# Performance work log

Hardware: AMD Instinct MI355X
Metric: run time of the kernel (lower is better)

## Reference

```python
import jax, jax.numpy as jnp
import numpy as np

B, T, D, H = 2, 2048, 1024, 16
DK = D // H  # 64


def setup_inputs() -> dict:
    key = jax.random.key(0)
    ks = jax.random.split(key, 13)
    s = 1.0 / np.sqrt(D)
    return {
        "x": jax.random.normal(ks[0], (B, T, D), jnp.float32),
        "Wq_w": jax.random.normal(ks[1], (D, D), jnp.float32) * s,
        "Wq_b": jax.random.normal(ks[2], (D,), jnp.float32) * 0.01,
        "Wk_w": jax.random.normal(ks[3], (D, D), jnp.float32) * s,
        "Wk_b": jax.random.normal(ks[4], (D,), jnp.float32) * 0.01,
        "Wv_w": jax.random.normal(ks[5], (D, D), jnp.float32) * s,
        "Wv_b": jax.random.normal(ks[6], (D,), jnp.float32) * 0.01,
        "Wo_w": jax.random.normal(ks[7], (D, D), jnp.float32) * s,
        "Wo_b": jax.random.normal(ks[8], (D,), jnp.float32) * 0.01,
        "qr": jax.random.normal(ks[9], (B, H, T, DK), jnp.float32),
        "qi": jax.random.normal(ks[10], (B, H, T, DK), jnp.float32),
        "kr": jax.random.normal(ks[11], (B, H, T, DK), jnp.float32),
        "ki": jax.random.normal(ks[12], (B, H, T, DK), jnp.float32),
    }


def _heads(y):
    # [B,T,D] -> [B,H,T,DK]
    return y.reshape(B, T, H, DK).transpose(0, 2, 1, 3)


def reference(x, Wq_w, Wq_b, Wk_w, Wk_b, Wv_w, Wv_b, Wo_w, Wo_b, qr, qi, kr, ki):
    Q = _heads(x @ Wq_w.T + Wq_b)
    K = _heads(x @ Wk_w.T + Wk_b)
    V = _heads(x @ Wv_w.T + Wv_b)
    # quantum noise: sin(atan2(imag, real))
    Q = Q + jnp.sin(jnp.arctan2(qi, qr))
    K = K + jnp.sin(jnp.arctan2(ki, kr))
    # Recursive fractal attention collapses: branches are identical and
    # deterministic, so (A1+A2)/2 == depth-0 attention at every level.
    scores = jnp.einsum("bhtd,bhsd->bhts", Q, K) / np.sqrt(DK).astype(np.float32)
    weights = jax.nn.softmax(scores, axis=-1)
    attn = jnp.einsum("bhts,bhsd->bhtd", weights, V)  # [B,H,T,DK]
    out = attn.transpose(0, 2, 1, 3).reshape(B, T, D)
    return out @ Wo_w.T + Wo_b
```

## Files before the change

### kernel.cpp

```cpp
#include <hip/hip_runtime.h>
#include <hip/hip_fp16.h>
#include <stdint.h>

typedef _Float16 half_t;
typedef _Float16 hf2 __attribute__((ext_vector_type(2)));
typedef _Float16 hf4 __attribute__((ext_vector_type(4)));
typedef _Float16 hf8 __attribute__((ext_vector_type(8)));
typedef float f32x16 __attribute__((ext_vector_type(16)));
typedef unsigned uint2_t __attribute__((ext_vector_type(2)));

#define LOG2E 1.4426950408889634f

__device__ __forceinline__ void gload16(const void* g, void* l) {
  __builtin_amdgcn_global_load_lds(
      (const __attribute__((address_space(1))) unsigned int*)g,
      (__attribute__((address_space(3))) unsigned int*)l, 16, 0, 0);
}

__device__ __forceinline__ unsigned packrtz(float a, float b) {
  auto h = __builtin_amdgcn_cvt_pkrtz(a, b);
  union { decltype(h) h2; unsigned u; } c;
  c.h2 = h;
  return c.u;
}

__device__ __forceinline__ float exp2fast(float x) {
#if __has_builtin(__builtin_amdgcn_exp2f)
  return __builtin_amdgcn_exp2f(x);
#else
  return exp2f(x);
#endif
}

__device__ __forceinline__ float psum2(unsigned pw, hf2 ones, float acc) {
#if __has_builtin(__builtin_amdgcn_fdot2)
  union { unsigned u; hf2 h; } c;
  c.u = pw;
  return __builtin_amdgcn_fdot2(c.h, ones, acc, false);
#else
  union { unsigned u; hf2 h; } c;
  c.u = pw;
  return acc + (float)c.h[0] + (float)c.h[1];
#endif
}

__global__ __launch_bounds__(256) void cvt_kernel(
    const float* __restrict__ x, const float* __restrict__ wq,
    const float* __restrict__ wk, const float* __restrict__ wv,
    const float* __restrict__ wo, half_t* __restrict__ xh,
    half_t* __restrict__ wh) {
  long e = ((long)blockIdx.x * 256 + threadIdx.x) * 16;
  const float* src;
  half_t* dst;
  if (e < 4194304L) {
    src = x + e;
    dst = xh + e;
  } else {
    long j = e - 4194304L;
    int w = (int)(j >> 20);
    long off = j & 1048575L;
    src = (w == 0 ? wq : w == 1 ? wk : w == 2 ? wv : wo) + off;
    dst = wh + ((long)w << 20) + off;
  }
  const float4* s4 = (const float4*)src;
  float4 f0 = s4[0], f1 = s4[1], f2 = s4[2], f3 = s4[3];
  hf8 o0 = {(half_t)f0.x, (half_t)f0.y, (half_t)f0.z, (half_t)f0.w,
            (half_t)f1.x, (half_t)f1.y, (half_t)f1.z, (half_t)f1.w};
  hf8 o1 = {(half_t)f2.x, (half_t)f2.y, (half_t)f2.z, (half_t)f2.w,
            (half_t)f3.x, (half_t)f3.y, (half_t)f3.z, (half_t)f3.w};
  *(hf8*)dst = o0;
  *(hf8*)(dst + 8) = o1;
}

template <int CUR>
__device__ __forceinline__ void gstep(bool stage, const half_t* __restrict__ A,
                                      const half_t* __restrict__ Bt, char* ldsb,
                                      int wid, int& goA, int& goB, int aof0,
                                      int aof1, int aof2, int aof3, int bof0,
                                      int bof1, int bof2, int bof3,
                                      f32x16 acc[2]) {
  if (stage) {
#pragma unroll
    for (int i = 0; i < 4; i++)
      gload16(A + goA + i * 32768,
              ldsb + (CUR ^ 1) * 16384 + i * 4096 + wid * 1024);
#pragma unroll
    for (int i = 0; i < 2; i++)
      gload16(Bt + goB + i * 32768,
              ldsb + 32768 + (CUR ^ 1) * 8192 + i * 4096 + wid * 1024);
    goA += 64;
    goB += 64;
  }
  constexpr int ca = CUR * 16384;
  constexpr int cb = 32768 + CUR * 8192;
#pragma unroll
  for (int kc = 0; kc < 4; kc++) {
    const int ao = (kc == 0 ? aof0 : kc == 1 ? aof1 : kc == 2 ? aof2 : aof3);
    const int bo = (kc == 0 ? bof0 : kc == 1 ? bof1 : kc == 2 ? bof2 : bof3);
    hf8 af0 = *(const hf8*)(ldsb + ca + ao);
    hf8 af1 = *(const hf8*)(ldsb + ca + ao + 4096);
    hf8 bf = *(const hf8*)(ldsb + cb + bo);
    acc[0] = __builtin_amdgcn_mfma_f32_32x32x16_f16(af0, bf, acc[0], 0, 0, 0);
    acc[1] = __builtin_amdgcn_mfma_f32_32x32x16_f16(af1, bf, acc[1], 0, 0, 0);
  }
  __syncthreads();
}

__device__ __forceinline__ void gemm_core(const half_t* __restrict__ A,
                                          const half_t* __restrict__ Bt,
                                          int m0, int n0, char* ldsb,
                                          f32x16 acc[2]) {
  const int tid = threadIdx.x;
  const int wid = tid >> 6;
  const int lane = tid & 63;
  const int l31 = lane & 31;
  const int hh = lane >> 5;
  const int wm = wid >> 1, wn = wid & 1;

#pragma unroll
  for (int mt = 0; mt < 2; mt++)
#pragma unroll
    for (int i = 0; i < 16; i++) acc[mt][i] = 0.f;

  const int rowb = tid >> 3;
  const int c16 = (tid & 7) ^ (rowb & 7);
  int goA = (m0 + rowb) * 1024 + c16 * 8;
  int goB = (n0 + rowb) * 1024 + c16 * 8;

  const int swz0 = (hh * 16) ^ ((l31 & 7) << 4);
  const int swz1 = (32 + hh * 16) ^ ((l31 & 7) << 4);
  const int swz2 = (64 + hh * 16) ^ ((l31 & 7) << 4);
  const int swz3 = (96 + hh * 16) ^ ((l31 & 7) << 4);
  const int arow = (wm * 64 + l31) * 128;
  const int brow = (wn * 32 + l31) * 128;
  const int aof0 = arow + swz0, aof1 = arow + swz1, aof2 = arow + swz2,
            aof3 = arow + swz3;
  const int bof0 = brow + swz0, bof1 = brow + swz1, bof2 = brow + swz2,
            bof3 = brow + swz3;

#pragma unroll
  for (int i = 0; i < 4; i++)
    gload16(A + goA + i * 32768, ldsb + i * 4096 + wid * 1024);
#pragma unroll
  for (int i = 0; i < 2; i++)
    gload16(Bt + goB + i * 32768, ldsb + 32768 + i * 4096 + wid * 1024);
  goA += 64;
  goB += 64;
  __syncthreads();

  for (int kp = 0; kp < 8; ++kp) {
    gstep<0>(true, A, Bt, ldsb, wid, goA, goB, aof0, aof1, aof2, aof3, bof0,
             bof1, bof2, bof3, acc);
    gstep<1>(kp < 7, A, Bt, ldsb, wid, goA, goB, aof0, aof1, aof2, aof3, bof0,
             bof1, bof2, bof3, acc);
  }
}

__global__ __launch_bounds__(256, 3) void proj_kernel(
    const half_t* __restrict__ xh, const half_t* __restrict__ wh,
    const float* __restrict__ bq, const float* __restrict__ bk,
    const float* __restrict__ bv, const float* __restrict__ qr,
    const float* __restrict__ qi, const float* __restrict__ kr,
    const float* __restrict__ ki, half_t* __restrict__ Qh,
    half_t* __restrict__ Kh, half_t* __restrict__ Vth) {
  __shared__ __align__(16) char ldsb[49152];
  const int z = blockIdx.z;
  const half_t* Bt = wh + (size_t)z * 1048576;
  const int m0 = blockIdx.x * 128, n0 = blockIdx.y * 64;
  f32x16 acc[2];
  gemm_core(xh, Bt, m0, n0, ldsb, acc);

  const int tid = threadIdx.x;
  const int wid = tid >> 6;
  const int lane = tid & 63;
  const int l31 = lane & 31;
  const int hh = lane >> 5;
  const int wm = wid >> 1, wn = wid & 1;
  const float* bias = (z == 0) ? bq : (z == 1) ? bk : bv;
  const float* nr = (z == 0) ? qr : kr;
  const float* ni = (z == 0) ? qi : ki;
  const float scale = (z == 0) ? (0.125f * LOG2E) : 1.0f;

  const int n = n0 + wn * 32 + l31;
  const float bsv = bias[n];
  const int hd = n >> 6, d = n & 63;
#pragma unroll
  for (int mt = 0; mt < 2; mt++) {
    const int mbase = m0 + wm * 64 + mt * 32;
    if (z == 2) {
#pragma unroll
      for (int g = 0; g < 4; g++) {
        const int m = mbase + 8 * g + 4 * hh;
        const int bb = m >> 11, tt = m & 2047;
        hf4 pk;
#pragma unroll
        for (int i2 = 0; i2 < 4; i2++)
          pk[i2] = (half_t)(acc[mt][4 * g + i2] + bsv);
        *(hf4*)(Vth + (((size_t)(bb * 16 + hd) * 64 + d) * 2048 + tt)) = pk;
      }
    } else {
      half_t* dstp = (z == 0) ? Qh : Kh;
#pragma unroll
      for (int r = 0; r < 16; r++) {
        const int m = mbase + (r & 3) + 8 * (r >> 2) + 4 * hh;
        const int bb = m >> 11, tt = m & 2047;
        const size_t idx = ((size_t)(bb * 16 + hd) * 2048 + tt) * 64 + d;
        float v = acc[mt][r] + bsv;
        const float a_ = nr[idx], b_ = ni[idx];
        v += b_ * rsqrtf(a_ * a_ + b_ * b_);
        dstp[idx] = (half_t)(v * scale);
      }
    }
  }
}

template <int CUR>
__device__ __forceinline__ void attn_tile_t(
    bool stage, const half_t* __restrict__ Kb, const half_t* __restrict__ Vb,
    char* base, int qw, int& gk0, int& gk1, int& gv0, int& gv1,
    const int kofs[4], const hf8 qf[4], const f32x16& zv, f32x16 ot[2],
    float& psAcc, hf2 ones) {
  if (stage) {
    gload16(Kb + gk0, base + (CUR ^ 1) * 8192 + qw * 1024);
    gload16(Kb + gk1, base + (CUR ^ 1) * 8192 + 4096 + qw * 1024);
    gload16(Vb + gv0, base + 16384 + (CUR ^ 1) * 8192 + qw * 1024);
    gload16(Vb + gv1, base + 16384 + (CUR ^ 1) * 8192 + 4096 + qw * 1024);
    gk0 += 4096;
    gk1 += 4096;
    gv0 += 64;
    gv1 += 64;
  }
#pragma unroll
  for (int kt = 0; kt < 2; kt++) {
    __builtin_amdgcn_s_setprio(1);
    f32x16 s = __builtin_amdgcn_mfma_f32_32x32x16_f16(
        *(const hf8*)(base + kofs[0] + CUR * 8192 + kt * 4096), qf[0], zv, 0, 0,
        0);
    s = __builtin_amdgcn_mfma_f32_32x32x16_f16(
        *(const hf8*)(base + kofs[1] + CUR * 8192 + kt * 4096), qf[1], s, 0, 0,
        0);
    s = __builtin_amdgcn_mfma_f32_32x32x16_f16(
        *(const hf8*)(base + kofs[2] + CUR * 8192 + kt * 4096), qf[2], s, 0, 0,
        0);
    s = __builtin_amdgcn_mfma_f32_32x32x16_f16(
        *(const hf8*)(base + kofs[3] + CUR * 8192 + kt * 4096), qf[3], s, 0, 0,
        0);
    __builtin_amdgcn_s_setprio(0);

    unsigned pw[8];
#pragma unroll
    for (int j = 0; j < 8; j++) {
      float p0 = exp2fast(s[2 * j]);
      float p1 = exp2fast(s[2 * j + 1]);
      pw[j] = packrtz(p0, p1);
      psAcc = psum2(pw[j], ones, psAcc);
    }

#pragma unroll
    for (int sub = 0; sub < 2; sub++) {
      const int kc = kt * 2 + sub;
      unsigned a0 = pw[sub * 4 + 0], a1 = pw[sub * 4 + 1];
      unsigned a2 = pw[sub * 4 + 2], a3 = pw[sub * 4 + 3];
      union { unsigned u[4]; hf8 v; } pu;
#if __has_builtin(__builtin_amdgcn_permlane32_swap)
      uint2_t r02 = __builtin_amdgcn_permlane32_swap(a0, a2, false, false);
      uint2_t r13 = __builtin_amdgcn_permlane32_swap(a1, a3, false, false);
      pu.u[0] = r02[0];
      pu.u[1] = r13[0];
      pu.u[2] = r02[1];
      pu.u[3] = r13[1];
#else
      const int hh_ = (threadIdx.x & 63) >> 5;
      unsigned x0 = __shfl_xor(a0, 32, 64), x1 = __shfl_xor(a1, 32, 64);
      unsigned x2 = __shfl_xor(a2, 32, 64), x3 = __shfl_xor(a3, 32, 64);
      pu.u[0] = hh_ ? x2 : a0;
      pu.u[1] = hh_ ? x3 : a1;
      pu.u[2] = hh_ ? a2 : x0;
      pu.u[3] = hh_ ? a3 : x1;
#endif
      __builtin_amdgcn_s_setprio(1);
#pragma unroll
      for (int dt = 0; dt < 2; dt++) {
        hf8 vf =
            *(const hf8*)(base + kofs[kc] + 16384 + CUR * 8192 + dt * 4096);
        ot[dt] =
            __builtin_amdgcn_mfma_f32_32x32x16_f16(vf, pu.v, ot[dt], 0, 0, 0);
      }
      __builtin_amdgcn_s_setprio(0);
    }
  }
  __syncthreads();
}

__global__ __launch_bounds__(512, 4) void attn_kernel(
    const half_t* __restrict__ Qh, const half_t* __restrict__ Kh,
    const half_t* __restrict__ Vth, half_t* __restrict__ ah) {
  __shared__ __align__(16) char smem[65536];
  const int tid = threadIdx.x, wid = tid >> 6, lane = tid & 63;
  const int l31 = lane & 31, hh = lane >> 5;
  const int qw = wid & 3, g = wid >> 2;
  const int lin = blockIdx.x;
  const int slot = lin >> 3;
  const int bh = (lin & 7) * 4 + (slot >> 4);
  const int qb = slot & 15;
  const int b = bh >> 4, hd = bh & 15;
  const int t = qb * 128 + qw * 32 + l31;

  char* base = smem + g * 32768;

  const half_t* qrow = Qh + ((size_t)bh * 2048 + t) * 64;
  hf8 qf[4];
#pragma unroll
  for (int kc = 0; kc < 4; kc++) qf[kc] = *(const hf8*)(qrow + kc * 16 + hh * 8);

  f32x16 ot[2];
#pragma unroll
  for (int dt = 0; dt < 2; dt++)
#pragma unroll
    for (int i = 0; i < 16; i++) ot[dt][i] = 0.f;
  f32x16 zv;
#pragma unroll
  for (int i = 0; i < 16; i++) zv[i] = 0.f;
  float psAcc = 0.f;
  const hf2 ones = {(_Float16)1.0f, (_Float16)1.0f};

  const half_t* Kb = Kh + (size_t)bh * 2048 * 64;
  const half_t* Vb = Vth + (size_t)bh * 64 * 2048;
  const int kvbase = g * 1024;

  int kofs[4];
#pragma unroll
  for (int kc = 0; kc < 4; kc++)
    kofs[kc] = l31 * 128 + ((kc * 32 + hh * 16) ^ ((l31 & 7) << 4));

  int gk0, gk1, gv0, gv1;
  {
    int c0 = qw * 64 + lane, c1 = 256 + qw * 64 + lane;
    int r0 = c0 >> 3, s0 = (c0 & 7) ^ (r0 & 7);
    int r1 = c1 >> 3, s1 = (c1 & 7) ^ (r1 & 7);
    gk0 = (kvbase + r0) * 64 + s0 * 8;
    gk1 = (kvbase + r1) * 64 + s1 * 8;
    gv0 = r0 * 2048 + kvbase + s0 * 8;
    gv1 = r1 * 2048 + kvbase + s1 * 8;
  }
  gload16(Kb + gk0, base + qw * 1024);
  gload16(Kb + gk1, base + 4096 + qw * 1024);
  gload16(Vb + gv0, base + 16384 + qw * 1024);
  gload16(Vb + gv1, base + 16384 + 4096 + qw * 1024);
  gk0 += 4096;
  gk1 += 4096;
  gv0 += 64;
  gv1 += 64;
  __syncthreads();

  for (int tp = 0; tp < 8; ++tp) {
    attn_tile_t<0>(true, Kb, Vb, base, qw, gk0, gk1, gv0, gv1, kofs, qf, zv,
                   ot, psAcc, ones);
    attn_tile_t<1>(tp < 7, Kb, Vb, base, qw, gk0, gk1, gv0, gv1, kofs, qf, zv,
                   ot, psAcc, ones);
  }

  const float lrun = psAcc + __shfl_xor(psAcc, 32, 64);

  float* cb = (float*)smem;
  float* lb = (float*)(smem + 32768);
  if (g == 1) {
#pragma unroll
    for (int dt = 0; dt < 2; dt++)
#pragma unroll
      for (int i = 0; i < 16; i++)
        cb[((qw * 2 + dt) * 16 + i) * 64 + lane] = ot[dt][i];
    lb[qw * 64 + lane] = lrun;
  }
  __syncthreads();
  if (g == 0) {
#pragma unroll
    for (int dt = 0; dt < 2; dt++)
#pragma unroll
      for (int i = 0; i < 16; i++)
        ot[dt][i] += cb[((qw * 2 + dt) * 16 + i) * 64 + lane];
    const float inv = 1.0f / (lrun + lb[qw * 64 + lane]);
    const size_t obase = ((size_t)b * 2048 + t) * 1024 + hd * 64;
#pragma unroll
    for (int dt = 0; dt < 2; dt++)
#pragma unroll
      for (int gg = 0; gg < 4; gg++) {
        hf4 pk;
#pragma unroll
        for (int i2 = 0; i2 < 4; i2++)
          pk[i2] = (half_t)(ot[dt][4 * gg + i2] * inv);
        *(hf4*)(ah + obase + dt * 32 + 8 * gg + 4 * hh) = pk;
      }
  }
}

__global__ __launch_bounds__(256, 3) void outproj_kernel(
    const half_t* __restrict__ ah, const half_t* __restrict__ woh,
    const float* __restrict__ bo, float* __restrict__ out) {
  __shared__ __align__(16) char ldsb[49152];
  const int m0 = blockIdx.x * 128, n0 = blockIdx.y * 64;
  f32x16 acc[2];
  gemm_core(ah, woh, m0, n0, ldsb, acc);
  const int tid = threadIdx.x, wid = tid >> 6, lane = tid & 63;
  const int l31 = lane & 31, hh = lane >> 5;
  const int wm = wid >> 1, wn = wid & 1;
  const int n = n0 + wn * 32 + l31;
  const float bsv = bo[n];
#pragma unroll
  for (int mt = 0; mt < 2; mt++) {
    const int mbase = m0 + wm * 64 + mt * 32;
#pragma unroll
    for (int r = 0; r < 16; r++) {
      const int m = mbase + (r & 3) + 8 * (r >> 2) + 4 * hh;
      out[(size_t)m * 1024 + n] = acc[mt][r] + bsv;
    }
  }
}

extern "C" void kernel_launch(void* const* d_in, const int* in_sizes, int n_in,
                              void* d_out, int out_size, void* d_ws,
                              size_t ws_size, hipStream_t stream) {
  const float* x = (const float*)d_in[0];
  const float* Wq = (const float*)d_in[1];
  const float* bq = (const float*)d_in[2];
  const float* Wk = (const float*)d_in[3];
  const float* bk = (const float*)d_in[4];
  const float* Wv = (const float*)d_in[5];
  const float* bv = (const float*)d_in[6];
  const float* Wo = (const float*)d_in[7];
  const float* bo = (const float*)d_in[8];
  const float* qr = (const float*)d_in[9];
  const float* qi = (const float*)d_in[10];
  const float* kr = (const float*)d_in[11];
  const float* ki = (const float*)d_in[12];
  float* out = (float*)d_out;

  char* ws = (char*)d_ws;
  half_t* xh = (half_t*)(ws);
  half_t* wh = (half_t*)(ws + 8388608);
  half_t* Qh = (half_t*)(ws + 16777216);
  half_t* Kh = (half_t*)(ws + 25165824);
  half_t* Vth = (half_t*)(ws + 33554432);
  half_t* ah = (half_t*)(ws + 41943040);

  cvt_kernel<<<dim3(2048), dim3(256), 0, stream>>>(x, Wq, Wk, Wv, Wo, xh, wh);
  proj_kernel<<<dim3(32, 16, 3), dim3(256), 0, stream>>>(
      xh, wh, bq, bk, bv, qr, qi, kr, ki, Qh, Kh, Vth);
  attn_kernel<<<dim3(512), dim3(512), 0, stream>>>(Qh, Kh, Vth, ah);
  outproj_kernel<<<dim3(32, 16), dim3(256), 0, stream>>>(ah, wh + 3 * 1048576,
                                                         bo, out);
}
```

Measured before the change: 108.3 us.

## Fuse Q/K/V projections into one kernel sharing the x tile

Replaces the three-way z-grid projection launch with a single kernel in which each block computes Q, K and V for the same 128x64 output tile, loading the x tile into LDS once and reusing it across three weight tiles. This cuts global traffic for x by a factor of three and reduces the block count. In exchange it drops the double-buffered gstep pipeline for a simple load-sync-compute loop, triples the accumulator registers (which may lower occupancy under the launch bounds), and yields only 512 blocks.

```diff
diff --git a/kernel.cpp b/kernel.cpp
--- a/kernel.cpp
+++ b/kernel.cpp
@@ -72,6 +72,132 @@
   *(hf8*)(dst + 8) = o1;
 }
 
+__global__ __launch_bounds__(256, 3) void proj_kernel(
+    const half_t* __restrict__ xh, const half_t* __restrict__ wh,
+    const float* __restrict__ bq, const float* __restrict__ bk,
+    const float* __restrict__ bv, const float* __restrict__ qr,
+    const float* __restrict__ qi, const float* __restrict__ kr,
+    const float* __restrict__ ki, half_t* __restrict__ Qh,
+    half_t* __restrict__ Kh, half_t* __restrict__ Vth) {
+  __shared__ __align__(16) char ldsb[40960];
+  const int m0 = blockIdx.x * 128, n0 = blockIdx.y * 64;
+  const int tid = threadIdx.x;
+  const int wid = tid >> 6;
+  const int lane = tid & 63;
+  const int l31 = lane & 31;
+  const int hh = lane >> 5;
+  const int wm = wid >> 1, wn = wid & 1;
+
+  f32x16 acc[3][2];
+#pragma unroll
+  for (int z = 0; z < 3; z++)
+#pragma unroll
+    for (int mt = 0; mt < 2; mt++)
+#pragma unroll
+      for (int i = 0; i < 16; i++) acc[z][mt][i] = 0.f;
+
+  const int rowb = tid >> 3;
+  const int c16 = (tid & 7) ^ (rowb & 7);
+  int goA = (m0 + rowb) * 1024 + c16 * 8;
+  int goB = (n0 + rowb) * 1024 + c16 * 8;
+
+  const int swz0 = (hh * 16) ^ ((l31 & 7) << 4);
+  const int swz1 = (32 + hh * 16) ^ ((l31 & 7) << 4);
+  const int swz2 = (64 + hh * 16) ^ ((l31 & 7) << 4);
+  const int swz3 = (96 + hh * 16) ^ ((l31 & 7) << 4);
+  const int arow = (wm * 64 + l31) * 128;
+  const int brow = 16384 + (wn * 32 + l31) * 128;
+  const int aof0 = arow + swz0, aof1 = arow + swz1, aof2 = arow + swz2,
+            aof3 = arow + swz3;
+  const int bof0 = brow + swz0, bof1 = brow + swz1, bof2 = brow + swz2,
+            bof3 = brow + swz3;
+
+  for (int kt = 0; kt < 16; ++kt) {
+#pragma unroll
+    for (int i = 0; i < 4; i++)
+      gload16(xh + goA + i * 32768, ldsb + i * 4096 + wid * 1024);
+#pragma unroll
+    for (int z = 0; z < 3; z++)
+#pragma unroll
+      for (int i = 0; i < 2; i++)
+        gload16(wh + z * 1048576 + goB + i * 32768,
+                ldsb + 16384 + z * 8192 + i * 4096 + wid * 1024);
+    goA += 64;
+    goB += 64;
+    __syncthreads();
+#pragma unroll
+    for (int kc = 0; kc < 4; kc++) {
+      const int ao = (kc == 0 ? aof0 : kc == 1 ? aof1 : kc == 2 ? aof2 : aof3);
+      const int bo = (kc == 0 ? bof0 : kc == 1 ? bof1 : kc == 2 ? bof2 : bof3);
+      hf8 af0 = *(const hf8*)(ldsb + ao);
+      hf8 af1 = *(const hf8*)(ldsb + ao + 4096);
+#pragma unroll
+      for (int z = 0; z < 3; z++) {
+        hf8 bf = *(const hf8*)(ldsb + bo + z * 8192);
+        acc[z][0] =
+            __builtin_amdgcn_mfma_f32_32x32x16_f16(af0, bf, acc[z][0], 0, 0, 0);
+        acc[z][1] =
+            __builtin_amdgcn_mfma_f32_32x32x16_f16(af1, bf, acc[z][1], 0, 0, 0);
+      }
+    }
+    __syncthreads();
+  }
+
+  const int n = n0 + wn * 32 + l31;
+  const int hd = n >> 6, d = n & 63;
+  {
+    const float bsv = bq[n];
+#pragma unroll
+    for (int mt = 0; mt < 2; mt++) {
+      const int mbase = m0 + wm * 64 + mt * 32;
+#pragma unroll
+      for (int r = 0; r < 16; r++) {
+        const int m = mbase + (r & 3) + 8 * (r >> 2) + 4 * hh;
+        const int bb = m >> 11, tt = m & 2047;
+        const size_t idx = ((size_t)(bb * 16 + hd) * 2048 + tt) * 64 + d;
+        float v = acc[0][mt][r] + bsv;
+        const float a_ = qr[idx], b_ = qi[idx];
+        v += b_ * rsqrtf(a_ * a_ + b_ * b_);
+        Qh[idx] = (half_t)(v * (0.125f * LOG2E));
+      }
+    }
+  }
+  {
+    const float bsv = bk[n];
+#pragma unroll
+    for (int mt = 0; mt < 2; mt++) {
+      const int mbase = m0 + wm * 64 + mt * 32;
+#pragma unroll
+      for (int r = 0; r < 16; r++) {
+        const int m = mbase + (r & 3) + 8 * (r >> 2) + 4 * hh;
+        const int bb = m >> 11, tt = m & 2047;
+        const size_t idx = ((size_t)(bb * 16 + hd) * 2048 + tt) * 64 + d;
+        float v = acc[1][mt][r] + bsv;
+        const float a_ = kr[idx], b_ = ki[idx];
+        v += b_ * rsqrtf(a_ * a_ + b_ * b_);
+        Kh[idx] = (half_t)v;
+      }
+    }
+  }
+  {
+    const float bsv = bv[n];
+#pragma unroll
+    for (int mt = 0; mt < 2; mt++) {
+      const int mbase = m0 + wm * 64 + mt * 32;
+#pragma unroll
+      for (int g = 0; g < 4; g++) {
+        const int m = mbase + 8 * g + 4 * hh;
+        const int bb = m >> 11, tt = m & 2047;
+        hf4 pk;
+#pragma unroll
+        for (int i2 = 0; i2 < 4; i2++)
+          pk[i2] = (half_t)(acc[2][mt][4 * g + i2] + bsv);
+        *(hf4*)(Vth + (((size_t)(bb * 16 + hd) * 64 + d) * 2048 + tt)) = pk;
+      }
+    }
+  }
+}
+
 template <int CUR>
 __device__ __forceinline__ void gstep(bool stage, const half_t* __restrict__ A,
                                       const half_t* __restrict__ Bt, char* ldsb,
@@ -153,64 +279,6 @@
              bof1, bof2, bof3, acc);
     gstep<1>(kp < 7, A, Bt, ldsb, wid, goA, goB, aof0, aof1, aof2, aof3, bof0,
              bof1, bof2, bof3, acc);
-  }
-}
-
-__global__ __launch_bounds__(256, 3) void proj_kernel(
-    const half_t* __restrict__ xh, const half_t* __restrict__ wh,
-    const float* __restrict__ bq, const float* __restrict__ bk,
-    const float* __restrict__ bv, const float* __restrict__ qr,
-    const float* __restrict__ qi, const float* __restrict__ kr,
-    const float* __restrict__ ki, half_t* __restrict__ Qh,
-    half_t* __restrict__ Kh, half_t* __restrict__ Vth) {
-  __shared__ __align__(16) char ldsb[49152];
-  const int z = blockIdx.z;
-  const half_t* Bt = wh + (size_t)z * 1048576;
-  const int m0 = blockIdx.x * 128, n0 = blockIdx.y * 64;
-  f32x16 acc[2];
-  gemm_core(xh, Bt, m0, n0, ldsb, acc);
-
-  const int tid = threadIdx.x;
-  const int wid = tid >> 6;
-  const int lane = tid & 63;
-  const int l31 = lane & 31;
-  const int hh = lane >> 5;
-  const int wm = wid >> 1, wn = wid & 1;
-  const float* bias = (z == 0) ? bq : (z == 1) ? bk : bv;
-  const float* nr = (z == 0) ? qr : kr;
-  const float* ni = (z == 0) ? qi : ki;
-  const float scale = (z == 0) ? (0.125f * LOG2E) : 1.0f;
-
-  const int n = n0 + wn * 32 + l31;
-  const float bsv = bias[n];
-  const int hd = n >> 6, d = n & 63;
-#pragma unroll
-  for (int mt = 0; mt < 2; mt++) {
-    const int mbase = m0 + wm * 64 + mt * 32;
-    if (z == 2) {
-#pragma unroll
-      for (int g = 0; g < 4; g++) {
-        const int m = mbase + 8 * g + 4 * hh;
-        const int bb = m >> 11, tt = m & 2047;
-        hf4 pk;
-#pragma unroll
-        for (int i2 = 0; i2 < 4; i2++)
-          pk[i2] = (half_t)(acc[mt][4 * g + i2] + bsv);
-        *(hf4*)(Vth + (((size_t)(bb * 16 + hd) * 64 + d) * 2048 + tt)) = pk;
-      }
-    } else {
-      half_t* dstp = (z == 0) ? Qh : Kh;
-#pragma unroll
-      for (int r = 0; r < 16; r++) {
-        const int m = mbase + (r & 3) + 8 * (r >> 2) + 4 * hh;
-        const int bb = m >> 11, tt = m & 2047;
-        const size_t idx = ((size_t)(bb * 16 + hd) * 2048 + tt) * 64 + d;
-        float v = acc[mt][r] + bsv;
-        const float a_ = nr[idx], b_ = ni[idx];
-        v += b_ * rsqrtf(a_ * a_ + b_ * b_);
-        dstp[idx] = (half_t)(v * scale);
-      }
-    }
   }
 }
 
@@ -444,7 +512,7 @@
   half_t* ah = (half_t*)(ws + 41943040);
 
   cvt_kernel<<<dim3(2048), dim3(256), 0, stream>>>(x, Wq, Wk, Wv, Wo, xh, wh);
-  proj_kernel<<<dim3(32, 16, 3), dim3(256), 0, stream>>>(
+  proj_kernel<<<dim3(32, 16), dim3(256), 0, stream>>>(
       xh, wh, bq, bk, bv, qr, qi, kr, ki, Qh, Kh, Vth);
   attn_kernel<<<dim3(512), dim3(512), 0, stream>>>(Qh, Kh, Vth, ah);
   outproj_kernel<<<dim3(32, 16), dim3(256), 0, stream>>>(ah, wh + 3 * 1048576,
```

Result: slower. 124.5 us (+14.9%).
